# Optimization experiments

Measured on AMD Instinct MI355X. Metric: run time of the kernel, lower is better.

The kernel has to match this reference:

```python
import jax, jax.numpy as jnp
import numpy as np

B, NODES, IN_DIM, OUT_DIM, CAPS, K, NUM_ROUTE = 32, 512, 256, 128, 16, 5, 3

def squash(s):
    # s: [..., out]; scale = |s|^2/(1+|s|^2), direction s/(|s|+eps)
    sn = jnp.sum(s * s, axis=-1, keepdims=True)
    return (sn / (1.0 + sn)) * s / (jnp.sqrt(sn) + 1e-8)

def setup_inputs() -> dict:
    key = jax.random.key(0)
    k1, k2, k3, k4 = jax.random.split(key, 4)
    return {
        "x": jax.random.normal(k1, (B, NODES, IN_DIM), jnp.float32),
        "contribution": jax.random.normal(k2, (B, NODES), jnp.float32),
        "W": jax.random.normal(k3, (K, IN_DIM, OUT_DIM), jnp.float32),
        "alpha": jax.random.normal(k4, (NODES, CAPS, K), jnp.float32),
    }

def reference(x, contribution, W, alpha):
    # per-node, per-capsule transform: sum_k alpha[n,c,k] * W[k,i,o] -> [nodes, caps, in, out]
    Wn = jnp.einsum('nck,kio->ncio', alpha, W)
    # prediction vectors u_hat: [B, caps, nodes, out]
    u_hat = jnp.einsum('bni,ncio->bcno', x, Wn)
    u_det = jax.lax.stop_gradient(u_hat)
    # routing logits b init from (detached) contribution: [B, caps, nodes, 1]
    b = jnp.broadcast_to(
        jax.lax.stop_gradient(contribution)[:, None, :, None],
        (x.shape[0], CAPS, x.shape[1], 1))
    for _ in range(NUM_ROUTE):
        c = jax.nn.softmax(b, axis=1)              # over capsule axis
        v = squash(jnp.sum(c * u_det, axis=2))     # [B, caps, out]
        b = b + jnp.einsum('bcno,bco->bcn', u_det, v)[..., None]
    c = jax.nn.softmax(b, axis=1)
    s = jnp.sum(c * u_hat, axis=2)                 # [B, caps, out] (non-detached)
    return squash(s)
```

## Files before the change

### kernel.cpp

```cpp
#include <hip/hip_runtime.h>
#include <math.h>

#define B_ 32
#define NODES_ 512
#define IN_ 256
#define OUT_ 128
#define CAPS_ 16
#define KW_ 5
#define M_ (B_*NODES_)
#define N_ (KW_*OUT_)
#define NCH 32

typedef __attribute__((ext_vector_type(8))) short short8;
typedef __attribute__((ext_vector_type(4))) float f32x4;

#define Y_BOFF   0
#define L_BOFF   41943040
#define V_BOFF   42991616
#define SP_BOFF  43253760
#define BT_SZ    (N_*IN_*2)

#define YPAD 644

__device__ __forceinline__ float b2f(unsigned short u) {
  union { unsigned int i; float f; } c; c.i = ((unsigned int)u) << 16; return c.f;
}
__device__ __forceinline__ unsigned short f2b(float f) {
  union { float f; unsigned int i; } c; c.f = f;
  unsigned int u = c.i;
  u += 0x7fffu + ((u >> 16) & 1u);
  return (unsigned short)(u >> 16);
}
__device__ __forceinline__ void async_load16(const void* g, void* l) {
  __builtin_amdgcn_global_load_lds(
      (const __attribute__((address_space(1))) unsigned int*)g,
      (__attribute__((address_space(3))) unsigned int*)l, 16, 0, 0);
}

__global__ __launch_bounds__(256) void conv_w(const float* __restrict__ W,
                                              unsigned short* __restrict__ bThi,
                                              unsigned short* __restrict__ bTlo) {
  int n = blockIdx.x;
  int i = threadIdx.x;
  int k = n >> 7, o = n & 127;
  float v = W[((size_t)k*IN_ + i)*OUT_ + o];
  unsigned short h = f2b(v);
  size_t dst = ((size_t)(i >> 3)*N_ + n)*8 + (i & 7);
  bThi[dst] = h;
  bTlo[dst] = f2b(v - b2f(h));
}

__global__ __launch_bounds__(512) void gemm_fn(const float* __restrict__ x,
                                               const unsigned short* __restrict__ bThi,
                                               const unsigned short* __restrict__ bTlo,
                                               float* __restrict__ y) {
  __shared__ float A_lds[8*64*4];
  __shared__ short Bh_lds[4*640*8];
  __shared__ short Bl_lds[4*640*8];
  const int t    = threadIdx.x;
  const int w    = t >> 6;
  const int lane = t & 63;
  const int lrow = lane & 15;
  const int lk   = lane >> 4;
  const int m0   = blockIdx.x * 64;
  const int wn0  = w * 80;
  const int arow = t >> 3;
  const int ac4  = t & 7;

  f32x4 acc[4][5];
  #pragma unroll
  for (int i=0;i<4;++i)
    #pragma unroll
    for (int j=0;j<5;++j) acc[i][j] = (f32x4){0.f,0.f,0.f,0.f};

  for (int kbi = 0; kbi < 8; ++kbi) {
    const int kb = kbi*32;
    const unsigned short* bh_src = bThi + (size_t)kbi*4*N_*8;
    const unsigned short* bl_src = bTlo + (size_t)kbi*4*N_*8;
    #pragma unroll
    for (int q=0; q<5; ++q) {
      int db = q*512 + w*64;
      async_load16(bh_src + (size_t)(db + lane)*8, &Bh_lds[db*8]);
      async_load16(bl_src + (size_t)(db + lane)*8, &Bl_lds[db*8]);
    }
    {
      float4 av = *(const float4*)(x + (size_t)(m0 + arow)*IN_ + kb + ac4*4);
      *(float4*)&A_lds[((ac4*64) + arow)*4] = av;
    }
    __syncthreads();

    short8 ah[4], al[4];
    #pragma unroll
    for (int mi=0; mi<4; ++mi) {
      int row = mi*16 + lrow;
      f32x4 a0 = *(const f32x4*)&A_lds[((2*lk  )*64 + row)*4];
      f32x4 a1 = *(const f32x4*)&A_lds[((2*lk+1)*64 + row)*4];
      #pragma unroll
      for (int j=0; j<8; ++j) {
        float f = (j < 4) ? a0[j] : a1[j-4];
        unsigned short h = f2b(f);
        ah[mi][j] = (short)h;
        al[mi][j] = (short)f2b(f - b2f(h));
      }
    }
    #pragma unroll
    for (int ni=0; ni<5; ++ni) {
      int nb = wn0 + ni*16 + lrow;
      short8 bh = *(const short8*)&Bh_lds[(lk*N_ + nb)*8];
      short8 bl = *(const short8*)&Bl_lds[(lk*N_ + nb)*8];
      #pragma unroll
      for (int mi=0; mi<4; ++mi) {
        acc[mi][ni] = __builtin_amdgcn_mfma_f32_16x16x32_bf16(bh, ah[mi], acc[mi][ni], 0, 0, 0);
        acc[mi][ni] = __builtin_amdgcn_mfma_f32_16x16x32_bf16(bh, al[mi], acc[mi][ni], 0, 0, 0);
        acc[mi][ni] = __builtin_amdgcn_mfma_f32_16x16x32_bf16(bl, ah[mi], acc[mi][ni], 0, 0, 0);
      }
    }
    __syncthreads();
  }

  #pragma unroll
  for (int mi=0; mi<4; ++mi) {
    int m = m0 + mi*16 + lrow;
    #pragma unroll
    for (int ni=0; ni<5; ++ni) {
      int nb = wn0 + ni*16 + lk*4;
      float4 o = {acc[mi][ni][0], acc[mi][ni][1], acc[mi][ni][2], acc[mi][ni][3]};
      *(float4*)(y + (size_t)m*N_ + nb) = o;
    }
  }
}

__global__ __launch_bounds__(256) void route_rs(const float* __restrict__ y,
                                                const float* __restrict__ alpha,
                                                const float* __restrict__ contrib,
                                                float* __restrict__ logits,
                                                const float* __restrict__ vin,
                                                float* __restrict__ s_part,
                                                int mode) {
  __shared__ __align__(16) float sh_y[16*YPAD];
  __shared__ __align__(16) float sh_v[16*132];
  __shared__ __align__(16) float sh_aT[16*80];
  __shared__ __align__(16) float sh_cwa[16*80];
  __shared__ float sh_cw[256];

  const int t  = threadIdx.x;
  const int ch = blockIdx.x;
  const int b  = blockIdx.y;
  const int n0 = ch*16;

  const float* ybase = y + ((size_t)(b*NODES_ + n0))*N_;
  float4 yst[10];
  #pragma unroll
  for (int q=0; q<10; ++q) yst[q] = *(const float4*)(ybase + (size_t)(t + q*256)*4);
  #pragma unroll
  for (int q=0; q<10; ++q) {
    int flat = (t + q*256)*4;
    int nd   = flat / 640;
    int rem  = flat - nd*640;
    *(float4*)&sh_y[nd*YPAD + rem] = yst[q];
  }
  const float* abase = alpha + (size_t)n0*CAPS_*KW_;
  for (int i = t; i < 320; i += 256) {
    float4 av = *(const float4*)(abase + i*4);
    int flat = i*4;
    int nd   = flat / 80;
    int rem  = flat - nd*80;
    #pragma unroll
    for (int e=0; e<4; ++e) {
      int r = rem + e;
      int c = r / 5;
      int k = r - c*5;
      sh_aT[nd*80 + k*16 + c] = av[e];
    }
  }
  if (mode >= 1) {
    const float* vbase = vin + (size_t)b*CAPS_*OUT_;
    #pragma unroll
    for (int q=0; q<2; ++q) {
      int flat = (t + q*256)*4;
      int c = flat >> 7, o = flat & 127;
      float4 vv = *(const float4*)(vbase + flat);
      *(float4*)&sh_v[c*132 + o] = vv;
    }
  } else {
    sh_cw[t] = 0.0625f;
    int nd = t >> 4, c = t & 15;
    logits[((size_t)b*CAPS_ + c)*NODES_ + n0 + nd] = contrib[(size_t)b*NODES_ + n0 + nd];
  }
  __syncthreads();

  if (mode >= 1) {
    const int nd = t >> 4, og = t & 15;
    float4 yq[5][2];
    #pragma unroll
    for (int k=0; k<5; ++k) {
      yq[k][0] = *(const float4*)&sh_y[nd*YPAD + k*128 + og*8];
      yq[k][1] = *(const float4*)&sh_y[nd*YPAD + k*128 + og*8 + 4];
    }
    float p[16];
    #pragma unroll
    for (int c=0;c<16;++c) p[c] = 0.f;
    #pragma unroll
    for (int cq=0; cq<4; ++cq) {
      float4 a5[5];
      #pragma unroll
      for (int k=0;k<5;++k) a5[k] = *(const float4*)&sh_aT[nd*80 + k*16 + cq*4];
      #pragma unroll
      for (int cl=0; cl<4; ++cl) {
        int c = cq*4 + cl;
        float4 v0 = *(const float4*)&sh_v[c*132 + og*8];
        float4 v1 = *(const float4*)&sh_v[c*132 + og*8 + 4];
        float d[5];
        #pragma unroll
        for (int k=0;k<5;++k) {
          d[k] = yq[k][0].x*v0.x + yq[k][0].y*v0.y + yq[k][0].z*v0.z + yq[k][0].w*v0.w
               + yq[k][1].x*v1.x + yq[k][1].y*v1.y + yq[k][1].z*v1.z + yq[k][1].w*v1.w;
        }
        p[c] += a5[0][cl]*d[0] + a5[1][cl]*d[1] + a5[2][cl]*d[2]
              + a5[3][cl]*d[3] + a5[4][cl]*d[4];
      }
    }
    float q8[8];
    #pragma unroll
    for (int j=0;j<8;++j) {
      float a = p[2*j], bb = p[2*j+1];
      float mine = (og & 1) ? bb : a;
      float othr = (og & 1) ? a  : bb;
      q8[j] = mine + __shfl_xor(othr, 1, 64);
    }
    float r4[4];
    #pragma unroll
    for (int j=0;j<4;++j) {
      float a = q8[2*j], bb = q8[2*j+1];
      float mine = (og & 2) ? bb : a;
      float othr = (og & 2) ? a  : bb;
      r4[j] = mine + __shfl_xor(othr, 2, 64);
    }
    float s2[2];
    #pragma unroll
    for (int j=0;j<2;++j) {
      float a = r4[2*j], bb = r4[2*j+1];
      float mine = (og & 4) ? bb : a;
      float othr = (og & 4) ? a  : bb;
      s2[j] = mine + __shfl_xor(othr, 4, 64);
    }
    float aa = s2[0], bb2 = s2[1];
    float mine4 = (og & 8) ? bb2 : aa;
    float othr4 = (og & 8) ? aa  : bb2;
    float fin = mine4 + __shfl_xor(othr4, 8, 64);

    float lold = logits[((size_t)b*CAPS_ + og)*NODES_ + n0 + nd];
    float newl = lold + fin;
    logits[((size_t)b*CAPS_ + og)*NODES_ + n0 + nd] = newl;
    float m = newl;
    m = fmaxf(m, __shfl_xor(m, 1, 64));
    m = fmaxf(m, __shfl_xor(m, 2, 64));
    m = fmaxf(m, __shfl_xor(m, 4, 64));
    m = fmaxf(m, __shfl_xor(m, 8, 64));
    float e = __expf(newl - m);
    float ssum = e;
    ssum += __shfl_xor(ssum, 1, 64);
    ssum += __shfl_xor(ssum, 2, 64);
    ssum += __shfl_xor(ssum, 4, 64);
    ssum += __shfl_xor(ssum, 8, 64);
    sh_cw[nd*16 + og] = e / ssum;
  }
  __syncthreads();

  #pragma unroll
  for (int i = t; i < 1280; i += 256) {
    int nd = i / 80;
    int c  = i & 15;
    sh_cwa[i] = sh_cw[nd*16 + c] * sh_aT[i];
  }
  __syncthreads();

  {
    const int oq = t & 31;
    const int cg = (t >> 5) & 1;
    const int ng = t >> 6;
    float acc[8][4];
    #pragma unroll
    for (int j=0;j<8;++j)
      #pragma unroll
      for (int oo=0;oo<4;++oo) acc[j][oo] = 0.f;

    #pragma unroll
    for (int ii=0; ii<4; ++ii) {
      int nd = ng + ii*4;
      #pragma unroll
      for (int k=0; k<5; ++k) {
        float4 yq  = *(const float4*)&sh_y[nd*YPAD + k*128 + oq*4];
        float4 ca0 = *(const float4*)&sh_cwa[nd*80 + k*16 + cg*8];
        float4 ca1 = *(const float4*)&sh_cwa[nd*80 + k*16 + cg*8 + 4];
        float cav[8] = {ca0.x,ca0.y,ca0.z,ca0.w,ca1.x,ca1.y,ca1.z,ca1.w};
        float yv[4]  = {yq.x,yq.y,yq.z,yq.w};
        #pragma unroll
        for (int j=0;j<8;++j)
          #pragma unroll
          for (int oo=0;oo<4;++oo)
            acc[j][oo] += cav[j]*yv[oo];
      }
    }
    __syncthreads();
    float* red = sh_y;
    #pragma unroll
    for (int j=0;j<8;++j) {
      float4 w4 = {acc[j][0], acc[j][1], acc[j][2], acc[j][3]};
      *(float4*)&red[(size_t)ng*2048 + (cg*8 + j)*128 + oq*4] = w4;
    }
    __syncthreads();
    const int c2 = t >> 4;
    const int o2 = (t & 15) * 8;
    float4 r0 = {0,0,0,0}, r1 = {0,0,0,0};
    #pragma unroll
    for (int g=0; g<4; ++g) {
      float4 q0 = *(const float4*)&red[(size_t)g*2048 + c2*128 + o2];
      float4 q1 = *(const float4*)&red[(size_t)g*2048 + c2*128 + o2 + 4];
      r0.x += q0.x; r0.y += q0.y; r0.z += q0.z; r0.w += q0.w;
      r1.x += q1.x; r1.y += q1.y; r1.z += q1.z; r1.w += q1.w;
    }
    float* spb = s_part + ((size_t)(b*NCH + ch)*CAPS_ + c2)*OUT_ + o2;
    *(float4*)(spb)     = r0;
    *(float4*)(spb + 4) = r1;
  }
}

__global__ __launch_bounds__(128) void squash_k(const float* __restrict__ s_part,
                                                float* __restrict__ out) {
  const int bc = blockIdx.x;
  const int o  = threadIdx.x;
  const int b = bc >> 4, c = bc & 15;
  const float* sp = s_part + ((size_t)(b*NCH)*CAPS_ + c)*OUT_ + o;
  float s = 0.f;
  #pragma unroll
  for (int ch=0; ch<NCH; ++ch) s += sp[(size_t)ch*CAPS_*OUT_];
  float ss = s*s;
  #pragma unroll
  for (int off=32; off>0; off>>=1) ss += __shfl_down(ss, off, 64);
  __shared__ float red[2];
  if ((o & 63) == 0) red[o>>6] = ss;
  __syncthreads();
  float sn = red[0] + red[1];
  float scale = (sn/(1.f+sn)) / (sqrtf(sn)+1e-8f);
  out[(size_t)bc*OUT_ + o] = scale*s;
}

extern "C" void kernel_launch(void* const* d_in, const int* in_sizes, int n_in,
                              void* d_out, int out_size, void* d_ws, size_t ws_size,
                              hipStream_t stream) {
  const float* x       = (const float*)d_in[0];
  const float* contrib = (const float*)d_in[1];
  const float* W       = (const float*)d_in[2];
  const float* alpha   = (const float*)d_in[3];
  float* out = (float*)d_out;
  char*  wsb = (char*)d_ws;

  float* y             = (float*)(wsb + Y_BOFF);
  float* logits        = (float*)(wsb + L_BOFF);
  float* v             = (float*)(wsb + V_BOFF);
  float* s_part        = (float*)(wsb + SP_BOFF);
  unsigned short* bThi = (unsigned short*)(wsb + SP_BOFF);
  unsigned short* bTlo = (unsigned short*)(wsb + SP_BOFF + BT_SZ);

  conv_w<<<N_, 256, 0, stream>>>(W, bThi, bTlo);
  gemm_fn<<<M_/64, 512, 0, stream>>>(x, bThi, bTlo, y);

  route_rs<<<dim3(NCH, B_), 256, 0, stream>>>(y, alpha, contrib, logits, v, s_part, 0);
  squash_k<<<B_*CAPS_, 128, 0, stream>>>(s_part, v);

  for (int it=0; it<3; ++it) {
    route_rs<<<dim3(NCH, B_), 256, 0, stream>>>(y, alpha, contrib, logits, v, s_part, 1);
    squash_k<<<B_*CAPS_, 128, 0, stream>>>(s_part, (it==2) ? out : v);
  }
}
```

Before: 129.1 us.

## Process two node chunks per routing block with register-prefetched y and transposed v layout

The routing kernel now handles two 16-node chunks per block, halving the grid. The second chunk's y tile is loaded into registers while the first chunk is being computed, to hide global-load latency. The v vectors are stored in LDS in an output-group-major layout so the per-thread v reads are laid out differently, presumably to cut bank conflicts. The costs are higher register pressure from the extra 10 float4 prefetch buffer and fewer blocks (512) to spread across the CUs.

New measurement: 129.3 us. No clear change (+0.2%).

```diff
diff --git a/kernel.cpp b/kernel.cpp
--- a/kernel.cpp
+++ b/kernel.cpp
@@ -21,6 +21,7 @@
 #define BT_SZ    (N_*IN_*2)
 
 #define YPAD 644
+#define VPAD 130
 
 __device__ __forceinline__ float b2f(unsigned short u) {
   union { unsigned int i; float f; } c; c.i = ((unsigned int)u) << 16; return c.f;
@@ -130,49 +131,23 @@
   }
 }
 
-__global__ __launch_bounds__(256) void route_rs(const float* __restrict__ y,
-                                                const float* __restrict__ alpha,
-                                                const float* __restrict__ contrib,
-                                                float* __restrict__ logits,
-                                                const float* __restrict__ vin,
-                                                float* __restrict__ s_part,
-                                                int mode) {
+__global__ __launch_bounds__(256) void route2(const float* __restrict__ y,
+                                              const float* __restrict__ alpha,
+                                              const float* __restrict__ contrib,
+                                              float* __restrict__ logits,
+                                              const float* __restrict__ vin,
+                                              float* __restrict__ s_part,
+                                              int mode) {
   __shared__ __align__(16) float sh_y[16*YPAD];
-  __shared__ __align__(16) float sh_v[16*132];
+  __shared__ __align__(16) float sh_v[16*VPAD];
   __shared__ __align__(16) float sh_aT[16*80];
   __shared__ __align__(16) float sh_cwa[16*80];
   __shared__ float sh_cw[256];
 
   const int t  = threadIdx.x;
-  const int ch = blockIdx.x;
+  const int cp = blockIdx.x;
   const int b  = blockIdx.y;
-  const int n0 = ch*16;
-
-  const float* ybase = y + ((size_t)(b*NODES_ + n0))*N_;
-  float4 yst[10];
-  #pragma unroll
-  for (int q=0; q<10; ++q) yst[q] = *(const float4*)(ybase + (size_t)(t + q*256)*4);
-  #pragma unroll
-  for (int q=0; q<10; ++q) {
-    int flat = (t + q*256)*4;
-    int nd   = flat / 640;
-    int rem  = flat - nd*640;
-    *(float4*)&sh_y[nd*YPAD + rem] = yst[q];
-  }
-  const float* abase = alpha + (size_t)n0*CAPS_*KW_;
-  for (int i = t; i < 320; i += 256) {
-    float4 av = *(const float4*)(abase + i*4);
-    int flat = i*4;
-    int nd   = flat / 80;
-    int rem  = flat - nd*80;
-    #pragma unroll
-    for (int e=0; e<4; ++e) {
-      int r = rem + e;
-      int c = r / 5;
-      int k = r - c*5;
-      sh_aT[nd*80 + k*16 + c] = av[e];
-    }
-  }
+
   if (mode >= 1) {
     const float* vbase = vin + (size_t)b*CAPS_*OUT_;
     #pragma unroll
@@ -180,149 +155,196 @@
       int flat = (t + q*256)*4;
       int c = flat >> 7, o = flat & 127;
       float4 vv = *(const float4*)(vbase + flat);
-      *(float4*)&sh_v[c*132 + o] = vv;
+      *(float4*)&sh_v[(o >> 3)*VPAD + c*8 + (o & 7)] = vv;
     }
   } else {
     sh_cw[t] = 0.0625f;
-    int nd = t >> 4, c = t & 15;
-    logits[((size_t)b*CAPS_ + c)*NODES_ + n0 + nd] = contrib[(size_t)b*NODES_ + n0 + nd];
-  }
-  __syncthreads();
-
-  if (mode >= 1) {
-    const int nd = t >> 4, og = t & 15;
-    float4 yq[5][2];
-    #pragma unroll
-    for (int k=0; k<5; ++k) {
-      yq[k][0] = *(const float4*)&sh_y[nd*YPAD + k*128 + og*8];
-      yq[k][1] = *(const float4*)&sh_y[nd*YPAD + k*128 + og*8 + 4];
-    }
-    float p[16];
-    #pragma unroll
-    for (int c=0;c<16;++c) p[c] = 0.f;
-    #pragma unroll
-    for (int cq=0; cq<4; ++cq) {
-      float4 a5[5];
-      #pragma unroll
-      for (int k=0;k<5;++k) a5[k] = *(const float4*)&sh_aT[nd*80 + k*16 + cq*4];
-      #pragma unroll
-      for (int cl=0; cl<4; ++cl) {
-        int c = cq*4 + cl;
-        float4 v0 = *(const float4*)&sh_v[c*132 + og*8];
-        float4 v1 = *(const float4*)&sh_v[c*132 + og*8 + 4];
-        float d[5];
-        #pragma unroll
-        for (int k=0;k<5;++k) {
-          d[k] = yq[k][0].x*v0.x + yq[k][0].y*v0.y + yq[k][0].z*v0.z + yq[k][0].w*v0.w
-               + yq[k][1].x*v1.x + yq[k][1].y*v1.y + yq[k][1].z*v1.z + yq[k][1].w*v1.w;
+  }
+
+  float4 yst[10], ynx[10];
+  {
+    const float* yb0 = y + ((size_t)(b*NODES_ + cp*32))*N_;
+    #pragma unroll
+    for (int q=0; q<10; ++q) yst[q] = *(const float4*)(yb0 + (size_t)(t + q*256)*4);
+  }
+
+  #pragma unroll
+  for (int hh = 0; hh < 2; ++hh) {
+    const int ch = cp*2 + hh;
+    const int n0 = ch*16;
+
+    #pragma unroll
+    for (int q=0; q<10; ++q) {
+      int flat = (t + q*256)*4;
+      int nd   = flat / 640;
+      int rem  = flat - nd*640;
+      float4 src = (hh == 0) ? yst[q] : ynx[q];
+      *(float4*)&sh_y[nd*YPAD + rem] = src;
+    }
+    {
+      const float* abase = alpha + (size_t)n0*CAPS_*KW_;
+      for (int i = t; i < 320; i += 256) {
+        float4 av = *(const float4*)(abase + i*4);
+        int flat = i*4;
+        int nd   = flat / 80;
+        int rem  = flat - nd*80;
+        #pragma unroll
+        for (int e=0; e<4; ++e) {
+          int r = rem + e;
+          int c = r / 5;
+          int k = r - c*5;
+          sh_aT[nd*80 + k*16 + c] = av[e];
         }
-        p[c] += a5[0][cl]*d[0] + a5[1][cl]*d[1] + a5[2][cl]*d[2]
-              + a5[3][cl]*d[3] + a5[4][cl]*d[4];
-      }
-    }
-    float q8[8];
-    #pragma unroll
-    for (int j=0;j<8;++j) {
-      float a = p[2*j], bb = p[2*j+1];
-      float mine = (og & 1) ? bb : a;
-      float othr = (og & 1) ? a  : bb;
-      q8[j] = mine + __shfl_xor(othr, 1, 64);
-    }
-    float r4[4];
-    #pragma unroll
-    for (int j=0;j<4;++j) {
-      float a = q8[2*j], bb = q8[2*j+1];
-      float mine = (og & 2) ? bb : a;
-      float othr = (og & 2) ? a  : bb;
-      r4[j] = mine + __shfl_xor(othr, 2, 64);
-    }
-    float s2[2];
-    #pragma unroll
-    for (int j=0;j<2;++j) {
-      float a = r4[2*j], bb = r4[2*j+1];
-      float mine = (og & 4) ? bb : a;
-      float othr = (og & 4) ? a  : bb;
-      s2[j] = mine + __shfl_xor(othr, 4, 64);
-    }
-    float aa = s2[0], bb2 = s2[1];
-    float mine4 = (og & 8) ? bb2 : aa;
-    float othr4 = (og & 8) ? aa  : bb2;
-    float fin = mine4 + __shfl_xor(othr4, 8, 64);
-
-    float lold = logits[((size_t)b*CAPS_ + og)*NODES_ + n0 + nd];
-    float newl = lold + fin;
-    logits[((size_t)b*CAPS_ + og)*NODES_ + n0 + nd] = newl;
-    float m = newl;
-    m = fmaxf(m, __shfl_xor(m, 1, 64));
-    m = fmaxf(m, __shfl_xor(m, 2, 64));
-    m = fmaxf(m, __shfl_xor(m, 4, 64));
-    m = fmaxf(m, __shfl_xor(m, 8, 64));
-    float e = __expf(newl - m);
-    float ssum = e;
-    ssum += __shfl_xor(ssum, 1, 64);
-    ssum += __shfl_xor(ssum, 2, 64);
-    ssum += __shfl_xor(ssum, 4, 64);
-    ssum += __shfl_xor(ssum, 8, 64);
-    sh_cw[nd*16 + og] = e / ssum;
-  }
-  __syncthreads();
-
-  #pragma unroll
-  for (int i = t; i < 1280; i += 256) {
-    int nd = i / 80;
-    int c  = i & 15;
-    sh_cwa[i] = sh_cw[nd*16 + c] * sh_aT[i];
-  }
-  __syncthreads();
-
-  {
-    const int oq = t & 31;
-    const int cg = (t >> 5) & 1;
-    const int ng = t >> 6;
-    float acc[8][4];
-    #pragma unroll
-    for (int j=0;j<8;++j)
-      #pragma unroll
-      for (int oo=0;oo<4;++oo) acc[j][oo] = 0.f;
-
-    #pragma unroll
-    for (int ii=0; ii<4; ++ii) {
-      int nd = ng + ii*4;
+      }
+    }
+    if (mode == 0) {
+      int nd = t >> 4, c = t & 15;
+      logits[((size_t)b*CAPS_ + c)*NODES_ + n0 + nd] = contrib[(size_t)b*NODES_ + n0 + nd];
+    }
+    __syncthreads();
+
+    if (hh == 0) {
+      const float* yb1 = y + ((size_t)(b*NODES_ + cp*32 + 16))*N_;
+      #pragma unroll
+      for (int q=0; q<10; ++q) ynx[q] = *(const float4*)(yb1 + (size_t)(t + q*256)*4);
+    }
+
+    if (mode >= 1) {
+      const int nd = t >> 4, og = t & 15;
+      float4 yq[5][2];
       #pragma unroll
       for (int k=0; k<5; ++k) {
-        float4 yq  = *(const float4*)&sh_y[nd*YPAD + k*128 + oq*4];
-        float4 ca0 = *(const float4*)&sh_cwa[nd*80 + k*16 + cg*8];
-        float4 ca1 = *(const float4*)&sh_cwa[nd*80 + k*16 + cg*8 + 4];
-        float cav[8] = {ca0.x,ca0.y,ca0.z,ca0.w,ca1.x,ca1.y,ca1.z,ca1.w};
-        float yv[4]  = {yq.x,yq.y,yq.z,yq.w};
-        #pragma unroll
-        for (int j=0;j<8;++j)
+        yq[k][0] = *(const float4*)&sh_y[nd*YPAD + k*128 + og*8];
+        yq[k][1] = *(const float4*)&sh_y[nd*YPAD + k*128 + og*8 + 4];
+      }
+      float p[16];
+      #pragma unroll
+      for (int c=0;c<16;++c) p[c] = 0.f;
+      #pragma unroll
+      for (int cq=0; cq<4; ++cq) {
+        float4 a5[5];
+        #pragma unroll
+        for (int k=0;k<5;++k) a5[k] = *(const float4*)&sh_aT[nd*80 + k*16 + cq*4];
+        #pragma unroll
+        for (int cl=0; cl<4; ++cl) {
+          int c = cq*4 + cl;
+          float4 v0 = *(const float4*)&sh_v[og*VPAD + c*8];
+          float4 v1 = *(const float4*)&sh_v[og*VPAD + c*8 + 4];
+          float d[5];
           #pragma unroll
-          for (int oo=0;oo<4;++oo)
-            acc[j][oo] += cav[j]*yv[oo];
-      }
-    }
-    __syncthreads();
-    float* red = sh_y;
-    #pragma unroll
-    for (int j=0;j<8;++j) {
-      float4 w4 = {acc[j][0], acc[j][1], acc[j][2], acc[j][3]};
-      *(float4*)&red[(size_t)ng*2048 + (cg*8 + j)*128 + oq*4] = w4;
-    }
-    __syncthreads();
-    const int c2 = t >> 4;
-    const int o2 = (t & 15) * 8;
-    float4 r0 = {0,0,0,0}, r1 = {0,0,0,0};
-    #pragma unroll
-    for (int g=0; g<4; ++g) {
-      float4 q0 = *(const float4*)&red[(size_t)g*2048 + c2*128 + o2];
-      float4 q1 = *(const float4*)&red[(size_t)g*2048 + c2*128 + o2 + 4];
-      r0.x += q0.x; r0.y += q0.y; r0.z += q0.z; r0.w += q0.w;
-      r1.x += q1.x; r1.y += q1.y; r1.z += q1.z; r1.w += q1.w;
-    }
-    float* spb = s_part + ((size_t)(b*NCH + ch)*CAPS_ + c2)*OUT_ + o2;
-    *(float4*)(spb)     = r0;
-    *(float4*)(spb + 4) = r1;
+          for (int k=0;k<5;++k) {
+            d[k] = yq[k][0].x*v0.x + yq[k][0].y*v0.y + yq[k][0].z*v0.z + yq[k][0].w*v0.w
+                 + yq[k][1].x*v1.x + yq[k][1].y*v1.y + yq[k][1].z*v1.z + yq[k][1].w*v1.w;
+          }
+          p[c] += a5[0][cl]*d[0] + a5[1][cl]*d[1] + a5[2][cl]*d[2]
+                + a5[3][cl]*d[3] + a5[4][cl]*d[4];
+        }
+      }
+      float q8[8];
+      #pragma unroll
+      for (int j=0;j<8;++j) {
+        float a = p[2*j], bb = p[2*j+1];
+        float mine = (og & 1) ? bb : a;
+        float othr = (og & 1) ? a  : bb;
+        q8[j] = mine + __shfl_xor(othr, 1, 64);
+      }
+      float r4[4];
+      #pragma unroll
+      for (int j=0;j<4;++j) {
+        float a = q8[2*j], bb = q8[2*j+1];
+        float mine = (og & 2) ? bb : a;
+        float othr = (og & 2) ? a  : bb;
+        r4[j] = mine + __shfl_xor(othr, 2, 64);
+      }
+      float s2[2];
+      #pragma unroll
+      for (int j=0;j<2;++j) {
+        float a = r4[2*j], bb = r4[2*j+1];
+        float mine = (og & 4) ? bb : a;
+        float othr = (og & 4) ? a  : bb;
+        s2[j] = mine + __shfl_xor(othr, 4, 64);
+      }
+      float aa = s2[0], bb2 = s2[1];
+      float mine4 = (og & 8) ? bb2 : aa;
+      float othr4 = (og & 8) ? aa  : bb2;
+      float fin = mine4 + __shfl_xor(othr4, 8, 64);
+
+      float lold = logits[((size_t)b*CAPS_ + og)*NODES_ + n0 + nd];
+      float newl = lold + fin;
+      logits[((size_t)b*CAPS_ + og)*NODES_ + n0 + nd] = newl;
+      float m = newl;
+      m = fmaxf(m, __shfl_xor(m, 1, 64));
+      m = fmaxf(m, __shfl_xor(m, 2, 64));
+      m = fmaxf(m, __shfl_xor(m, 4, 64));
+      m = fmaxf(m, __shfl_xor(m, 8, 64));
+      float e = __expf(newl - m);
+      float ssum = e;
+      ssum += __shfl_xor(ssum, 1, 64);
+      ssum += __shfl_xor(ssum, 2, 64);
+      ssum += __shfl_xor(ssum, 4, 64);
+      ssum += __shfl_xor(ssum, 8, 64);
+      sh_cw[nd*16 + og] = e / ssum;
+    }
+    __syncthreads();
+
+    #pragma unroll
+    for (int i = t; i < 1280; i += 256) {
+      int nd = i / 80;
+      int c  = i & 15;
+      sh_cwa[i] = sh_cw[nd*16 + c] * sh_aT[i];
+    }
+    __syncthreads();
+
+    {
+      const int oq = t & 31;
+      const int cg = (t >> 5) & 1;
+      const int ng = t >> 6;
+      float acc[8][4];
+      #pragma unroll
+      for (int j=0;j<8;++j)
+        #pragma unroll
+        for (int oo=0;oo<4;++oo) acc[j][oo] = 0.f;
+
+      #pragma unroll
+      for (int ii=0; ii<4; ++ii) {
+        int nd = ng + ii*4;
+        #pragma unroll
+        for (int k=0; k<5; ++k) {
+          float4 yq  = *(const float4*)&sh_y[nd*YPAD + k*128 + oq*4];
+          float4 ca0 = *(const float4*)&sh_cwa[nd*80 + k*16 + cg*8];
+          float4 ca1 = *(const float4*)&sh_cwa[nd*80 + k*16 + cg*8 + 4];
+          float cav[8] = {ca0.x,ca0.y,ca0.z,ca0.w,ca1.x,ca1.y,ca1.z,ca1.w};
+          float yv[4]  = {yq.x,yq.y,yq.z,yq.w};
+          #pragma unroll
+          for (int j=0;j<8;++j)
+            #pragma unroll
+            for (int oo=0;oo<4;++oo)
+              acc[j][oo] += cav[j]*yv[oo];
+        }
+      }
+      __syncthreads();
+      float* red = sh_y;
+      #pragma unroll
+      for (int j=0;j<8;++j) {
+        float4 w4 = {acc[j][0], acc[j][1], acc[j][2], acc[j][3]};
+        *(float4*)&red[(size_t)ng*2048 + (cg*8 + j)*128 + oq*4] = w4;
+      }
+      __syncthreads();
+      const int c2 = t >> 4;
+      const int o2 = (t & 15) * 8;
+      float4 r0 = {0,0,0,0}, r1 = {0,0,0,0};
+      #pragma unroll
+      for (int g=0; g<4; ++g) {
+        float4 q0 = *(const float4*)&red[(size_t)g*2048 + c2*128 + o2];
+        float4 q1 = *(const float4*)&red[(size_t)g*2048 + c2*128 + o2 + 4];
+        r0.x += q0.x; r0.y += q0.y; r0.z += q0.z; r0.w += q0.w;
+        r1.x += q1.x; r1.y += q1.y; r1.z += q1.z; r1.w += q1.w;
+      }
+      float* spb = s_part + ((size_t)(b*NCH + ch)*CAPS_ + c2)*OUT_ + o2;
+      *(float4*)(spb)     = r0;
+      *(float4*)(spb + 4) = r1;
+    }
+    __syncthreads();
   }
 }
 
@@ -366,11 +388,11 @@
   conv_w<<<N_, 256, 0, stream>>>(W, bThi, bTlo);
   gemm_fn<<<M_/64, 512, 0, stream>>>(x, bThi, bTlo, y);
 
-  route_rs<<<dim3(NCH, B_), 256, 0, stream>>>(y, alpha, contrib, logits, v, s_part, 0);
+  route2<<<dim3(NCH/2, B_), 256, 0, stream>>>(y, alpha, contrib, logits, v, s_part, 0);
   squash_k<<<B_*CAPS_, 128, 0, stream>>>(s_part, v);
 
   for (int it=0; it<3; ++it) {
-    route_rs<<<dim3(NCH, B_), 256, 0, stream>>>(y, alpha, contrib, logits, v, s_part, 1);
+    route2<<<dim3(NCH/2, B_), 256, 0, stream>>>(y, alpha, contrib, logits, v, s_part, 1);
     squash_k<<<B_*CAPS_, 128, 0, stream>>>(s_part, (it==2) ? out : v);
   }
 }
```
